# Optimization experiments

Hardware: AMD Instinct MI355X
Metric: run time of the kernel (lower is better)

Reference implementation:

```python
import jax, jax.numpy as jnp
from jax import lax
import numpy as np

B, S, I, H, L = 128, 256, 512, 768, 2  # batch, seq, input, hidden, layers


def _lstm_dir(x_seq, Wx, bx, Wh, bh, h0, c0):
    """Run one LSTM direction over x_seq [B,S,D]. Gate order f,i,g,o (as torch.chunk)."""
    xg = jnp.einsum('bsd,dg->bsg', x_seq, Wx) + bx  # precompute input projections [B,S,4H]

    def step(carry, xg_t):
        h, c = carry
        gates = xg_t + h @ Wh + bh
        f, i, g, o = jnp.split(gates, 4, axis=-1)
        c = jax.nn.sigmoid(f) * c + jax.nn.sigmoid(i) * jnp.tanh(g)
        h = jax.nn.sigmoid(o) * jnp.tanh(c)
        return (h, c), h

    (h, c), hs = lax.scan(step, (h0, c0), jnp.swapaxes(xg, 0, 1))  # scan over time
    return jnp.swapaxes(hs, 0, 1), h, c  # outputs [B,S,H], final h, c


def _mk_params(key, in_dim, hid):
    k1, k2 = jax.random.split(key)
    s_x = 1.0 / np.sqrt(in_dim)
    s_h = 1.0 / np.sqrt(hid)
    Wx = jax.random.uniform(k1, (in_dim, 4 * hid), jnp.float32, -s_x, s_x)
    bx = jnp.zeros((4 * hid,), jnp.float32)
    Wh = jax.random.uniform(k2, (hid, 4 * hid), jnp.float32, -s_h, s_h)
    bh = jnp.zeros((4 * hid,), jnp.float32)
    return Wx, bx, Wh, bh


def setup_inputs() -> dict:
    key = jax.random.key(0)
    ks = jax.random.split(key, 5)
    x = jax.random.normal(ks[0], (B, S, I), jnp.float32)
    out = {'x': x}
    names = [('f0', I), ('f1', H), ('b0', I), ('b1', H)]
    for k, (tag, in_dim) in zip(ks[1:], names):
        Wx, bx, Wh, bh = _mk_params(k, in_dim, H)
        out[f'Wx_{tag}'] = Wx
        out[f'bx_{tag}'] = bx
        out[f'Wh_{tag}'] = Wh
        out[f'bh_{tag}'] = bh
    return out


def reference(x, Wx_f0, bx_f0, Wh_f0, bh_f0, Wx_f1, bx_f1, Wh_f1, bh_f1,
              Wx_b0, bx_b0, Wh_b0, bh_b0, Wx_b1, bx_b1, Wh_b1, bh_b1):
    b = x.shape[0]
    z = jnp.zeros((b, H), x.dtype)
    fwd_params = [(Wx_f0, bx_f0, Wh_f0, bh_f0), (Wx_f1, bx_f1, Wh_f1, bh_f1)]
    bwd_params = [(Wx_b0, bx_b0, Wh_b0, bh_b0), (Wx_b1, bx_b1, Wh_b1, bh_b1)]

    inp_f = x
    inp_b = jnp.flip(x, axis=1)  # backward direction consumes reversed sequence
    h_f, c_f, h_b, c_b = [], [], [], []
    for layer in range(L):
        inp_f, hf, cf = _lstm_dir(inp_f, *fwd_params[layer], z, z)
        h_f.append(hf); c_f.append(cf)
        inp_b, hb, cb = _lstm_dir(inp_b, *bwd_params[layer], z, z)
        h_b.append(hb); c_b.append(cb)

    output = jnp.concatenate([inp_f, jnp.flip(inp_b, axis=1)], axis=-1)  # [B,S,2H]
    h_n = jnp.stack(h_f + h_b, axis=0)  # [2L,B,H], forward layers then backward
    c_n = jnp.stack(c_f + c_b, axis=0)
    return output, h_n, c_n
```

## Files before the change

### kernel.cpp

```cpp
#include <hip/hip_runtime.h>

#define BATCH 128
#define SEQ   256
#define IDIM  512
#define HDIM  768
#define G4    3072
#define BK    32
#define LSTR  72

typedef __bf16 bf16;
typedef __bf16 bf16x8 __attribute__((ext_vector_type(8)));
typedef float  f32x4  __attribute__((ext_vector_type(4)));

__device__ __forceinline__ float sigf(float x){ return 1.f/(1.f + __expf(-x)); }
__device__ __forceinline__ float tanhf_(float x){ return 1.f - 2.f/(1.f + __expf(2.f*x)); }


__global__ void convert_x_k(const float* __restrict__ x, bf16* __restrict__ xb){
  long i = ((long)blockIdx.x*256 + threadIdx.x)*8;
  float4 a = *(const float4*)(x+i);
  float4 b = *(const float4*)(x+i+4);
  bf16x8 o;
  o[0]=(bf16)a.x; o[1]=(bf16)a.y; o[2]=(bf16)a.z; o[3]=(bf16)a.w;
  o[4]=(bf16)b.x; o[5]=(bf16)b.y; o[6]=(bf16)b.z; o[7]=(bf16)b.w;
  *(bf16x8*)(xb+i) = o;
}

__global__ void build_wt_k(const float* __restrict__ wx, const float* __restrict__ wh,
                           bf16* __restrict__ wt, int k0, int kc){
  int idx = blockIdx.x*256 + threadIdx.x;
  int c = idx / kc;
  int k = idx - c*kc;
  int g = (c >> 4) & 3;
  int j = ((c >> 6) << 4) | (c & 15);
  int oc = g*HDIM + j;
  float v = (k < k0) ? wx[(long)k*G4 + oc] : wh[(long)(k-k0)*G4 + oc];
  wt[idx] = (bf16)v;
}

__global__ void build_bias_k(const float* __restrict__ bx, const float* __restrict__ bh,
                             float* __restrict__ bc){
  int c = blockIdx.x*256 + threadIdx.x;
  int g = (c >> 4) & 3;
  int j = ((c >> 6) << 4) | (c & 15);
  int oc = g*HDIM + j;
  bc[c] = bx[oc] + bh[oc];
}


struct CellP {
  const bf16* seg0;
  const bf16* seg1;
  const bf16* wt;
  const float* bias;
  float* cbuf;
  bf16*  hout;
  float* out;
  float* hn;
  float* cn;
  int s0stride, k0, kc, active;
};
struct StepArgs { CellP cell[4]; };

__launch_bounds__(256, 2)
__global__ void lstm_step_k(StepArgs args){
  const CellP p = args.cell[blockIdx.x / 48];
  if (!p.active) return;
  int r = blockIdx.x % 48;
  int mtile = r / 24, ntile = r % 24;
  int tid = threadIdx.x;
  int lane = tid & 63, wave = tid >> 6;
  int wm = wave >> 1, wn = wave & 1;
  int l15 = lane & 15, q = lane >> 4;

  __shared__ __align__(16) bf16 lds_a[64*LSTR];
  __shared__ __align__(16) bf16 lds_b[128*LSTR];

  f32x4 acc[2][4] = {};

  int arow = tid >> 2;
  int akp  = (tid & 3) << 3;
  int brow = tid >> 1;
  int bkp  = (tid & 1) << 4;

  int ga   = mtile*64 + arow;
  int ncol = ntile*128 + brow;
  const bf16* wrow  = p.wt + (long)ncol * p.kc;
  const bf16* aseg0 = p.seg0 + (long)ga * p.s0stride;
  const bf16* aseg1 = p.seg1 + ga * HDIM;

  int nk = p.kc / BK;
  for (int kb = 0; kb < nk; ++kb){
    int k  = kb*BK;
    int ka = k + akp;
    const bf16* asrc = (ka < p.k0) ? (aseg0 + ka) : (aseg1 + (ka - p.k0));
    bf16x8 av  = *(const bf16x8*)asrc;
    bf16x8 bv0 = *(const bf16x8*)(wrow + k + bkp);
    bf16x8 bv1 = *(const bf16x8*)(wrow + k + bkp + 8);
    __syncthreads();
    *(bf16x8*)(lds_a + arow*LSTR + akp)     = av;
    *(bf16x8*)(lds_b + brow*LSTR + bkp)     = bv0;
    *(bf16x8*)(lds_b + brow*LSTR + bkp + 8) = bv1;
    __syncthreads();
    bf16x8 af[2], bfr[4];
#pragma unroll
    for (int mi=0; mi<2; ++mi)
      af[mi] = *(const bf16x8*)(lds_a + (wm*32 + mi*16 + l15)*LSTR + q*8);
#pragma unroll
    for (int ni=0; ni<4; ++ni)
      bfr[ni] = *(const bf16x8*)(lds_b + (wn*64 + ni*16 + l15)*LSTR + q*8);
#pragma unroll
    for (int mi=0; mi<2; ++mi)
#pragma unroll
      for (int ni=0; ni<4; ++ni)
        acc[mi][ni] = __builtin_amdgcn_mfma_f32_16x16x32_bf16(af[mi], bfr[ni], acc[mi][ni], 0, 0, 0);
  }

  int colb = ntile*128 + wn*64;
  int j = ((colb >> 6) << 4) | l15;
  float bias4[4];
#pragma unroll
  for (int ni=0; ni<4; ++ni) bias4[ni] = p.bias[colb + ni*16 + l15];

#pragma unroll
  for (int mi=0; mi<2; ++mi){
    int b0 = mtile*64 + wm*32 + mi*16 + q*4;
#pragma unroll
    for (int rg=0; rg<4; ++rg){
      int b = b0 + rg;
      float fg = acc[mi][0][rg] + bias4[0];
      float ig = acc[mi][1][rg] + bias4[1];
      float gg = acc[mi][2][rg] + bias4[2];
      float og = acc[mi][3][rg] + bias4[3];
      float co = p.cbuf[b*HDIM + j];
      float cn = sigf(fg)*co + sigf(ig)*tanhf_(gg);
      float h  = sigf(og)*tanhf_(cn);
      p.cbuf[b*HDIM + j] = cn;
      p.hout[b*HDIM + j] = (bf16)h;
      if (p.out) p.out[(long)b*(SEQ*2*HDIM) + j] = h;
      if (p.hn){ p.hn[b*HDIM + j] = h; p.cn[b*HDIM + j] = cn; }
    }
  }
}


extern "C" void kernel_launch(void* const* d_in, const int* in_sizes, int n_in,
                              void* d_out, int out_size, void* d_ws, size_t ws_size,
                              hipStream_t stream){
  (void)in_sizes; (void)n_in; (void)out_size; (void)ws_size;
  const float* x = (const float*)d_in[0];
  const float* Wx[4]; const float* bxp[4]; const float* Whp[4]; const float* bhp[4];
  for (int t=0; t<4; ++t){
    Wx[t]  = (const float*)d_in[1 + 4*t];
    bxp[t] = (const float*)d_in[2 + 4*t];
    Whp[t] = (const float*)d_in[3 + 4*t];
    bhp[t] = (const float*)d_in[4 + 4*t];
  }
  const int tag[4] = {0, 2, 1, 3};
  const int k0c[4] = {IDIM, IDIM, HDIM, HDIM};
  const int kcc[4] = {IDIM+HDIM, IDIM+HDIM, 2*HDIM, 2*HDIM};

  char* ws = (char*)d_ws;
  size_t off = 0;
  auto take = [&](size_t bytes)->char*{ char* pp = ws + off; off += (bytes + 255) & ~(size_t)255; return pp; };

  bf16* xb = (bf16*)take((size_t)BATCH*SEQ*IDIM*2);
  bf16* wt[4];    for (int c=0;c<4;++c) wt[c]   = (bf16*)take((size_t)G4*kcc[c]*2);
  float* bias[4]; for (int c=0;c<4;++c) bias[c] = (float*)take((size_t)G4*4);
  bf16* hseq[4];  for (int c=0;c<4;++c) hseq[c] = (bf16*)take((size_t)SEQ*BATCH*HDIM*2);
  bf16* zeros = (bf16*)take((size_t)BATCH*HDIM*2);
  float* cbuf[4]; for (int c=0;c<4;++c) cbuf[c] = (float*)take((size_t)BATCH*HDIM*4);

  size_t zlen = (size_t)BATCH*HDIM*2 + 4*(size_t)BATCH*HDIM*4;
  hipMemsetAsync(zeros, 0, zlen, stream);

  convert_x_k<<<dim3((BATCH*SEQ*IDIM)/(8*256)), dim3(256), 0, stream>>>(x, xb);
  for (int c=0;c<4;++c)
    build_wt_k<<<dim3((G4*kcc[c])/256), dim3(256), 0, stream>>>(Wx[tag[c]], Whp[tag[c]], wt[c], k0c[c], kcc[c]);
  for (int c=0;c<4;++c)
    build_bias_k<<<dim3(G4/256), dim3(256), 0, stream>>>(bxp[tag[c]], bhp[tag[c]], bias[c]);

  float* outF = (float*)d_out;
  float* hnF  = outF + (size_t)BATCH*SEQ*2*HDIM;
  float* cnF  = hnF + (size_t)4*BATCH*HDIM;
  const int hnidx[4] = {0, 2, 1, 3};
  const size_t BH = (size_t)BATCH*HDIM;

  for (int kk=0; kk<=SEQ; ++kk){
    StepArgs A;
    for (int c=0; c<2; ++c){
      CellP& P = A.cell[c];
      int t = (kk < SEQ) ? kk : 0;
      P.active = (kk < SEQ);
      int ts = (c==0) ? t : (SEQ-1-t);
      P.seg0 = xb + (size_t)ts*IDIM;
      P.s0stride = SEQ*IDIM;
      P.k0 = k0c[c]; P.kc = kcc[c];
      P.seg1 = (t==0) ? zeros : (hseq[c] + (size_t)(t-1)*BH);
      P.wt = wt[c]; P.bias = bias[c]; P.cbuf = cbuf[c];
      P.hout = hseq[c] + (size_t)t*BH;
      P.out = nullptr;
      if (P.active && t == SEQ-1){ P.hn = hnF + hnidx[c]*BH; P.cn = cnF + hnidx[c]*BH; }
      else { P.hn = nullptr; P.cn = nullptr; }
    }
    for (int c=2; c<4; ++c){
      CellP& P = A.cell[c];
      int t = (kk >= 1) ? (kk-1) : 0;
      P.active = (kk >= 1);
      P.seg0 = hseq[c-2] + (size_t)t*BH;
      P.s0stride = HDIM;
      P.k0 = k0c[c]; P.kc = kcc[c];
      P.seg1 = (t==0) ? zeros : (hseq[c] + (size_t)(t-1)*BH);
      P.wt = wt[c]; P.bias = bias[c]; P.cbuf = cbuf[c];
      P.hout = hseq[c] + (size_t)t*BH;
      P.out = (c==2) ? (outF + (size_t)t*2*HDIM)
                     : (outF + (size_t)(SEQ-1-t)*2*HDIM + HDIM);
      if (P.active && t == SEQ-1){ P.hn = hnF + hnidx[c]*BH; P.cn = cnF + hnidx[c]*BH; }
      else { P.hn = nullptr; P.cn = nullptr; }
    }
    lstm_step_k<<<dim3(192), dim3(256), 0, stream>>>(A);
  }
}
```

Baseline: 8.057 ms.

## Pipeline LSTM step GEMM with 4-stage direct-to-LDS async loads and swizzle

Replaces the register-staged global-to-LDS copy, which used two barriers per k-block, with global_load_lds direct-to-LDS transfers into a 4-buffer ring prefetched 3 blocks ahead. It uses explicit vmcnt waits and a single barrier per iteration. The padded LDS layout is replaced by an XOR swizzle on 16-byte chunks to avoid bank conflicts. The aim is to hide global-load latency in the per-timestep recurrent GEMM, at the cost of more LDS (4 stages) and fragile hand-written waitcnt and ordering logic.

```diff
diff --git a/kernel.cpp b/kernel.cpp
--- a/kernel.cpp
+++ b/kernel.cpp
@@ -6,7 +6,6 @@
 #define HDIM  768
 #define G4    3072
 #define BK    32
-#define LSTR  72
 
 typedef __bf16 bf16;
 typedef __bf16 bf16x8 __attribute__((ext_vector_type(8)));
@@ -14,6 +13,12 @@
 
 __device__ __forceinline__ float sigf(float x){ return 1.f/(1.f + __expf(-x)); }
 __device__ __forceinline__ float tanhf_(float x){ return 1.f - 2.f/(1.f + __expf(2.f*x)); }
+
+__device__ __forceinline__ void gll16(const bf16* g, bf16* l){
+  __builtin_amdgcn_global_load_lds(
+      (const __attribute__((address_space(1))) void*)g,
+      (__attribute__((address_space(3))) void*)l, 16, 0, 0);
+}
 
 
 __global__ void convert_x_k(const float* __restrict__ x, bf16* __restrict__ xb){
@@ -69,51 +74,76 @@
   int r = blockIdx.x % 48;
   int mtile = r / 24, ntile = r % 24;
   int tid = threadIdx.x;
-  int lane = tid & 63, wave = tid >> 6;
-  int wm = wave >> 1, wn = wave & 1;
+  int lane = tid & 63, w = tid >> 6;
+  int wm = w >> 1, wn = w & 1;
   int l15 = lane & 15, q = lane >> 4;
 
-  __shared__ __align__(16) bf16 lds_a[64*LSTR];
-  __shared__ __align__(16) bf16 lds_b[128*LSTR];
+  __shared__ __align__(16) bf16 sA[4][64*BK];
+  __shared__ __align__(16) bf16 sB[4][128*BK];
 
   f32x4 acc[2][4] = {};
 
-  int arow = tid >> 2;
-  int akp  = (tid & 3) << 3;
-  int brow = tid >> 1;
-  int bkp  = (tid & 1) << 4;
-
-  int ga   = mtile*64 + arow;
-  int ncol = ntile*128 + brow;
-  const bf16* wrow  = p.wt + (long)ncol * p.kc;
-  const bf16* aseg0 = p.seg0 + (long)ga * p.s0stride;
-  const bf16* aseg1 = p.seg1 + ga * HDIM;
+  int rl  = lane >> 2;
+  int lch = (lane & 3) ^ ((lane >> 3) & 3);
+
+  int ra = w*16 + rl;
+  int ga = mtile*64 + ra;
+  const bf16* a0 = p.seg0 + (long)ga * p.s0stride + lch*8;
+  const bf16* a1 = p.seg1 + (long)ga * HDIM + lch*8 - p.k0;
+
+  long ncol0 = (long)ntile*128;
+  const bf16* b0p = p.wt + (ncol0 + w*16     + rl) * (long)p.kc + lch*8;
+  const bf16* b1p = p.wt + (ncol0 + (w+4)*16 + rl) * (long)p.kc + lch*8;
+
+  bf16* sAw  = &sA[0][0] + w*512;
+  bf16* sBw0 = &sB[0][0] + w*512;
+  bf16* sBw1 = &sB[0][0] + (w+4)*512;
 
   int nk = p.kc / BK;
+  int k0 = p.k0;
+
+#pragma unroll
+  for (int pb = 0; pb < 3; ++pb){
+    const bf16* as = (pb*BK < k0) ? (a0 + pb*BK) : (a1 + pb*BK);
+    gll16(as,          sAw  + pb*(64*BK));
+    gll16(b0p + pb*BK, sBw0 + pb*(128*BK));
+    gll16(b1p + pb*BK, sBw1 + pb*(128*BK));
+  }
+
+  int psel = (q ^ ((l15 >> 1) & 3)) * 8;
+
   for (int kb = 0; kb < nk; ++kb){
-    int k  = kb*BK;
-    int ka = k + akp;
-    const bf16* asrc = (ka < p.k0) ? (aseg0 + ka) : (aseg1 + (ka - p.k0));
-    bf16x8 av  = *(const bf16x8*)asrc;
-    bf16x8 bv0 = *(const bf16x8*)(wrow + k + bkp);
-    bf16x8 bv1 = *(const bf16x8*)(wrow + k + bkp + 8);
-    __syncthreads();
-    *(bf16x8*)(lds_a + arow*LSTR + akp)     = av;
-    *(bf16x8*)(lds_b + brow*LSTR + bkp)     = bv0;
-    *(bf16x8*)(lds_b + brow*LSTR + bkp + 8) = bv1;
-    __syncthreads();
+    int rem = nk - 1 - kb;
+    if (rem >= 2)      asm volatile("s_waitcnt vmcnt(6)" ::: "memory");
+    else if (rem == 1) asm volatile("s_waitcnt vmcnt(3)" ::: "memory");
+    else               asm volatile("s_waitcnt vmcnt(0)" ::: "memory");
+    __builtin_amdgcn_s_barrier();
+    __builtin_amdgcn_sched_barrier(0);
+
+    int nb = kb + 3;
+    if (nb < nk){
+      int buf = nb & 3;
+      const bf16* as = (nb*BK < k0) ? (a0 + nb*BK) : (a1 + nb*BK);
+      gll16(as,          sAw  + buf*(64*BK));
+      gll16(b0p + nb*BK, sBw0 + buf*(128*BK));
+      gll16(b1p + nb*BK, sBw1 + buf*(128*BK));
+    }
+
+    const bf16* A  = sA[kb & 3];
+    const bf16* Bm = sB[kb & 3];
     bf16x8 af[2], bfr[4];
 #pragma unroll
-    for (int mi=0; mi<2; ++mi)
-      af[mi] = *(const bf16x8*)(lds_a + (wm*32 + mi*16 + l15)*LSTR + q*8);
-#pragma unroll
-    for (int ni=0; ni<4; ++ni)
-      bfr[ni] = *(const bf16x8*)(lds_b + (wn*64 + ni*16 + l15)*LSTR + q*8);
-#pragma unroll
-    for (int mi=0; mi<2; ++mi)
-#pragma unroll
-      for (int ni=0; ni<4; ++ni)
+    for (int mi = 0; mi < 2; ++mi)
+      af[mi] = *(const bf16x8*)(A + (wm*32 + mi*16 + l15)*BK + psel);
+#pragma unroll
+    for (int ni = 0; ni < 4; ++ni)
+      bfr[ni] = *(const bf16x8*)(Bm + (wn*64 + ni*16 + l15)*BK + psel);
+#pragma unroll
+    for (int mi = 0; mi < 2; ++mi)
+#pragma unroll
+      for (int ni = 0; ni < 4; ++ni)
         acc[mi][ni] = __builtin_amdgcn_mfma_f32_16x16x32_bf16(af[mi], bfr[ni], acc[mi][ni], 0, 0, 0);
+    __builtin_amdgcn_sched_barrier(0);
   }
 
   int colb = ntile*128 + wn*64;
```

Measured after the change: 7.597 ms. -5.7%, faster.
